# Kernel tuning notes

Hardware: AMD Instinct MI355X
Metric: run time of the kernel (lower is better)

Reference implementation:

```python
import jax, jax.numpy as jnp
import numpy as np

B, S, IN, IN2, H = 512, 256, 300, 300, 512
FN = 3  # filter_num


def setup_inputs() -> dict:
    key = jax.random.key(0)
    ks = jax.random.split(key, 16)
    def n(k, shape, scale=0.05):
        return jax.random.normal(k, shape, dtype=jnp.float32) * scale
    return {
        "x": jax.random.normal(ks[0], (B, S, IN), dtype=jnp.float32),
        "W_in": n(ks[1], (IN, IN2)), "b_in": n(ks[2], (IN2,)),
        "Wih": n(ks[3], (IN2, 4 * H)), "Whh": n(ks[4], (H, 4 * H)),
        "bih": n(ks[5], (4 * H,)), "bhh": n(ks[6], (4 * H,)),
        "Q": n(ks[7], (H, IN2)), "R": n(ks[8], (IN2, H)),
        "Wc3": n(ks[9], (FN, 1, 3, H)), "bc3": n(ks[10], (FN,)),
        "Wc4": n(ks[11], (FN, 1, 4, H)), "bc4": n(ks[12], (FN,)),
        "Wc5": n(ks[13], (FN, 1, 5, H)), "bc5": n(ks[14], (FN,)),
        "W_lin": n(ks[15], (3 * FN, 2)), "b_lin": jnp.zeros((2,), jnp.float32),
    }


def reference(x, W_in, b_in, Wih, Whh, bih, bhh, Q, R,
              Wc3, bc3, Wc4, bc4, Wc5, bc5, W_lin, b_lin):
    # input projection: [B,S,IN] -> [B,S,IN2]
    xin = jnp.tanh(x @ W_in + b_in)
    xs = jnp.swapaxes(xin, 0, 1)  # [S,B,IN2] for scan
    bsz = x.shape[0]
    h0 = jnp.zeros((bsz, H), x.dtype)
    c0 = jnp.zeros((bsz, H), x.dtype)

    def step(carry, xt):
        ht, Ct = carry
        # mogrify, mog_iterations=2: i=1 odd updates x, i=2 even updates h
        xt = 2.0 * jax.nn.sigmoid(ht @ Q) * xt
        ht = 2.0 * jax.nn.sigmoid(xt @ R) * ht
        gates = xt @ Wih + bih + ht @ Whh + bhh  # [B,4H]
        i, f, g, o = jnp.split(gates, 4, axis=1)
        Ct = jax.nn.sigmoid(f) * Ct + jax.nn.sigmoid(i) * jnp.tanh(g)
        ht = jax.nn.sigmoid(o) * jnp.tanh(Ct)
        return (ht, Ct), ht

    _, hs = jax.lax.scan(step, (h0, c0), xs)  # [S,B,H]
    hmap = jnp.swapaxes(hs, 0, 1)[:, None, :, :]  # [B,1,S,H]

    feats = []
    for w, b in ((Wc3, bc3), (Wc4, bc4), (Wc5, bc5)):
        y = jax.lax.conv_general_dilated(
            hmap, w, (1, 1), 'VALID',
            dimension_numbers=('NCHW', 'OIHW', 'NCHW'))
        y = jax.nn.relu(y + b[None, :, None, None])  # [B,FN,S-fsz+1,1]
        feats.append(jnp.max(y, axis=(2, 3)))  # global max pool -> [B,FN]
    cat = jnp.concatenate(feats, axis=1)  # [B, 3*FN]
    # dropout is identity at inference
    return cat @ W_lin + b_lin  # [B,2]
```

## Files before the change

### kernel.cpp

```cpp
#include <hip/hip_runtime.h>

#define DI __device__ __forceinline__

typedef __attribute__((ext_vector_type(4))) float  f32x4;
typedef __attribute__((ext_vector_type(8))) short  s16x8;
typedef __attribute__((ext_vector_type(8))) __bf16 bf16x8;

constexpr int S_   = 256;
constexpr int B_   = 512;
constexpr int H_   = 512;
constexpr int KP_  = 320;
constexpr int ALD_ = 832;
constexpr int NRING = 34;
constexpr int NWG  = 256;
constexpr size_t HSLOT = 512 * 512;

constexpr size_t OFF_XIN = 0;
constexpr size_t SZ_XIN  = (size_t)S_ * B_ * KP_ * 2;
constexpr size_t OFF_U   = OFF_XIN + SZ_XIN;
constexpr size_t SZ_U    = (size_t)B_ * S_ * 64 * 4;
constexpr size_t OFF_HS  = OFF_U + SZ_U;
constexpr size_t SZ_HS   = (size_t)NRING * HSLOT * 2;
constexpr size_t OFF_ACT = OFF_HS + SZ_HS;
constexpr size_t SZ_ACT  = (size_t)B_ * ALD_ * 2;
constexpr size_t OFF_HFP = OFF_ACT + SZ_ACT;
constexpr size_t SZ_HFP  = (size_t)B_ * H_ * 4;
constexpr size_t OFF_WPT = OFF_HFP + SZ_HFP;
constexpr size_t SZ_WPT  = (size_t)320 * 320 * 2;
constexpr size_t OFF_QPT = OFF_WPT + SZ_WPT;
constexpr size_t SZ_QPT  = (size_t)320 * 512 * 2;
constexpr size_t OFF_RPT = OFF_QPT + SZ_QPT;
constexpr size_t SZ_RPT  = (size_t)512 * 320 * 2;
constexpr size_t OFF_WGT = OFF_RPT + SZ_RPT;
constexpr size_t SZ_WGT  = (size_t)2048 * 832 * 2;
constexpr size_t OFF_BG  = OFF_WGT + SZ_WGT;
constexpr size_t SZ_BG   = 2048 * 4;
constexpr size_t OFF_VT  = OFF_BG + SZ_BG;
constexpr size_t SZ_VT   = (size_t)64 * 512 * 2;
constexpr size_t OFF_BAR = OFF_VT + SZ_VT;
constexpr size_t SZ_BAR  = 4096;
constexpr size_t WS_NEED = OFF_BAR + SZ_BAR;

DI unsigned short f2bf(float x) {
  unsigned int u = __float_as_uint(x);
  unsigned int r = (u + 0x7FFFu + ((u >> 16) & 1u)) >> 16;
  return (unsigned short)r;
}
DI float bf2f(unsigned short h) { return __uint_as_float(((unsigned int)h) << 16); }

DI float sigm(float x) {
  float e = __builtin_amdgcn_exp2f(x * -1.44269504088896f);
  return __builtin_amdgcn_rcpf(1.0f + e);
}
DI float tanh_(float x) {
  x = fminf(fmaxf(x, -15.0f), 15.0f);
  float e = __builtin_amdgcn_exp2f(x * 2.88539008177793f);
  return (e - 1.0f) * __builtin_amdgcn_rcpf(e + 1.0f);
}
DI bf16x8 asbf(s16x8 v) { return __builtin_bit_cast(bf16x8, v); }

DI unsigned long long ld_sys_u64(const void* p) {
  return __hip_atomic_load((const unsigned long long*)p, __ATOMIC_RELAXED,
                           __HIP_MEMORY_SCOPE_SYSTEM);
}
DI void st_sys_u64(void* p, unsigned long long v) {
  __hip_atomic_store((unsigned long long*)p, v, __ATOMIC_RELAXED,
                     __HIP_MEMORY_SCOPE_SYSTEM);
}
template<int N> DI void wait_vm() {
  asm volatile("s_waitcnt vmcnt(%0)" :: "n"(N) : "memory");
}

struct a16x8 { unsigned long long lo, hi; };
DI a16x8 ldA(const unsigned short* p) {
  a16x8 r; r.lo = ld_sys_u64(p); r.hi = ld_sys_u64(p + 4); return r;
}
DI void stA_lds(short* dst, a16x8 v) {
  *(unsigned long long*)dst = v.lo; *(unsigned long long*)(dst + 4) = v.hi;
}

template<int NK>
DI void gemm_sys(const unsigned short* Ab, int lda,
                 const unsigned short* Bb, int ldb,
                 short* sA, short* sB, f32x4 acc[2][2])
{
  const int tid  = threadIdx.x;
  const int lane = tid & 63;
  const int w = tid >> 6, wm = w >> 1, wn = w & 1;
  const unsigned short* ga = Ab + (tid >> 2) * lda + (tid & 3) * 8;
  const unsigned short* gb = Bb + (tid >> 2) * ldb + (tid & 3) * 8;
  const int arow0 = (wm * 32 + (lane & 15)) * 32 + (lane >> 4) * 8;
  const int brow0 = (wn * 32 + (lane & 15)) * 32 + (lane >> 4) * 8;

  a16x8 a0 = ldA(ga), a1 = {};
  s16x8 b0 = *(const s16x8*)gb, b1 = {};
  if (NK > 1) { a1 = ldA(ga + 32); b1 = *(const s16x8*)(gb + 32); }
  stA_lds(&sA[tid * 8], a0);
  *(s16x8*)&sB[tid * 8] = b0;
  __syncthreads();
  #pragma unroll
  for (int k = 0; k < NK; ++k) {
    const int cur = (k & 1) * 2048;
    if (k + 2 < NK) {
      if ((k & 1) == 0) { a0 = ldA(ga + (k + 2) * 32); b0 = *(const s16x8*)(gb + (k + 2) * 32); }
      else              { a1 = ldA(ga + (k + 2) * 32); b1 = *(const s16x8*)(gb + (k + 2) * 32); }
    }
    s16x8 A0 = *(const s16x8*)&sA[cur + arow0];
    s16x8 A1 = *(const s16x8*)&sA[cur + arow0 + 16 * 32];
    s16x8 B0 = *(const s16x8*)&sB[cur + brow0];
    s16x8 B1 = *(const s16x8*)&sB[cur + brow0 + 16 * 32];
    acc[0][0] = __builtin_amdgcn_mfma_f32_16x16x32_bf16(asbf(A0), asbf(B0), acc[0][0], 0, 0, 0);
    acc[0][1] = __builtin_amdgcn_mfma_f32_16x16x32_bf16(asbf(A0), asbf(B1), acc[0][1], 0, 0, 0);
    acc[1][0] = __builtin_amdgcn_mfma_f32_16x16x32_bf16(asbf(A1), asbf(B0), acc[1][0], 0, 0, 0);
    acc[1][1] = __builtin_amdgcn_mfma_f32_16x16x32_bf16(asbf(A1), asbf(B1), acc[1][1], 0, 0, 0);
    if (k + 1 < NK) {
      const int nxt = ((k + 1) & 1) * 2048;
      if ((k & 1) == 0) { stA_lds(&sA[nxt + tid * 8], a1); *(s16x8*)&sB[nxt + tid * 8] = b1; }
      else              { stA_lds(&sA[nxt + tid * 8], a0); *(s16x8*)&sB[nxt + tid * 8] = b0; }
    }
    __syncthreads();
  }
}

template<int NK, int KREAL>
DI void gemm_f32A(const float* Af, int lda,
                  const unsigned short* Bb, int ldb,
                  short* sA, short* sB, f32x4 acc[2][2])
{
  const int tid  = threadIdx.x;
  const int lane = tid & 63;
  const int w = tid >> 6, wm = w >> 1, wn = w & 1;
  const float* ga = Af + (tid >> 2) * lda;
  const int cseg  = (tid & 3) * 8;
  const unsigned short* gb = Bb + (tid >> 2) * ldb + (tid & 3) * 8;
  const int arow0 = (wm * 32 + (lane & 15)) * 32 + (lane >> 4) * 8;
  const int brow0 = (wn * 32 + (lane & 15)) * 32 + (lane >> 4) * 8;

  auto loadA = [&](int k) -> s16x8 {
    s16x8 r;
    const int c0 = k * 32 + cseg;
    if (c0 + 8 <= KREAL) {
      float4 f0 = *(const float4*)(ga + c0);
      float4 f1 = *(const float4*)(ga + c0 + 4);
      r[0] = (short)f2bf(f0.x); r[1] = (short)f2bf(f0.y);
      r[2] = (short)f2bf(f0.z); r[3] = (short)f2bf(f0.w);
      r[4] = (short)f2bf(f1.x); r[5] = (short)f2bf(f1.y);
      r[6] = (short)f2bf(f1.z); r[7] = (short)f2bf(f1.w);
    } else {
      #pragma unroll
      for (int j = 0; j < 8; ++j) {
        float x = (c0 + j < KREAL) ? ga[c0 + j] : 0.0f;
        r[j] = (short)f2bf(x);
      }
    }
    return r;
  };

  s16x8 va = loadA(0);
  s16x8 vb = *(const s16x8*)gb;
  *(s16x8*)&sA[tid * 8] = va;
  *(s16x8*)&sB[tid * 8] = vb;
  __syncthreads();
  for (int k = 0; k < NK; ++k) {
    const int cur = (k & 1) * 2048;
    if (k + 1 < NK) {
      va = loadA(k + 1);
      vb = *(const s16x8*)(gb + (k + 1) * 32);
    }
    s16x8 a0 = *(const s16x8*)&sA[cur + arow0];
    s16x8 a1 = *(const s16x8*)&sA[cur + arow0 + 16 * 32];
    s16x8 b0 = *(const s16x8*)&sB[cur + brow0];
    s16x8 b1 = *(const s16x8*)&sB[cur + brow0 + 16 * 32];
    acc[0][0] = __builtin_amdgcn_mfma_f32_16x16x32_bf16(asbf(a0), asbf(b0), acc[0][0], 0, 0, 0);
    acc[0][1] = __builtin_amdgcn_mfma_f32_16x16x32_bf16(asbf(a0), asbf(b1), acc[0][1], 0, 0, 0);
    acc[1][0] = __builtin_amdgcn_mfma_f32_16x16x32_bf16(asbf(a1), asbf(b0), acc[1][0], 0, 0, 0);
    acc[1][1] = __builtin_amdgcn_mfma_f32_16x16x32_bf16(asbf(a1), asbf(b1), acc[1][1], 0, 0, 0);
    if (k + 1 < NK) {
      const int nxt = ((k + 1) & 1) * 2048;
      *(s16x8*)&sA[nxt + tid * 8] = va;
      *(s16x8*)&sB[nxt + tid * 8] = vb;
    }
    __syncthreads();
  }
}

template<typename F>
DI void epiloop(f32x4 acc[2][2], F&& f) {
  const int lane = threadIdx.x & 63;
  const int w = threadIdx.x >> 6, wm = w >> 1, wn = w & 1;
  #pragma unroll
  for (int mi = 0; mi < 2; ++mi)
    #pragma unroll
    for (int ni = 0; ni < 2; ++ni)
      #pragma unroll
      for (int r = 0; r < 4; ++r) {
        const int rowl = wm * 32 + mi * 16 + (lane >> 4) * 4 + r;
        const int coll = wn * 32 + ni * 16 + (lane & 15);
        f(rowl, coll, acc[mi][ni][r]);
      }
}

DI void pack_store_tile(const unsigned short* lds16, unsigned short* dstbase, int ldd) {
  const unsigned long long* l64 = (const unsigned long long*)lds16;
  #pragma unroll
  for (int it = 0; it < 4; ++it) {
    const int i = it * 256 + threadIdx.x;
    const int row = i >> 4, q = i & 15;
    st_sys_u64(dstbase + row * ldd + q * 4, l64[row * 16 + q]);
  }
}

__global__ void k_prep_wpt(const float* __restrict__ Wi, unsigned short* __restrict__ WpT) {
  int i = blockIdx.x * 256 + threadIdx.x;
  if (i >= 320 * 320) return;
  int n = i / 320, k = i % 320;
  float v = (n < 300 && k < 300) ? Wi[k * 300 + n] : 0.0f;
  WpT[i] = f2bf(v);
}
__global__ void k_prep_qpt(const float* __restrict__ Q, unsigned short* __restrict__ QpT) {
  int i = blockIdx.x * 256 + threadIdx.x;
  if (i >= 320 * 512) return;
  int n = i >> 9, k = i & 511;
  float v = (n < 300) ? Q[k * 300 + n] : 0.0f;
  QpT[i] = f2bf(v);
}
__global__ void k_prep_rpt(const float* __restrict__ R, unsigned short* __restrict__ RpT) {
  int i = blockIdx.x * 256 + threadIdx.x;
  if (i >= 512 * 320) return;
  int n = i / 320, k = i % 320;
  float v = (k < 300) ? R[k * 512 + n] : 0.0f;
  RpT[i] = f2bf(v);
}
__global__ void k_prep_wgt(const float* __restrict__ Wih, const float* __restrict__ Whh,
                           unsigned short* __restrict__ WgT) {
  int i = blockIdx.x * 256 + threadIdx.x;
  if (i >= 2048 * 832) return;
  int np = i / 832, k = i % 832;
  int c = np >> 2, g = np & 3, col = g * 512 + c;
  float v = 0.0f;
  if (k < 300) v = Wih[k * 2048 + col];
  else if (k >= 320) v = Whh[(k - 320) * 2048 + col];
  WgT[i] = f2bf(v);
}
__global__ void k_prep_bg(const float* __restrict__ bih, const float* __restrict__ bhh,
                          float* __restrict__ bg) {
  int i = blockIdx.x * 256 + threadIdx.x;
  if (i >= 2048) return;
  int c = i >> 2, g = i & 3, col = g * 512 + c;
  bg[i] = bih[col] + bhh[col];
}
__global__ void k_prep_vt(const float* __restrict__ Wc3, const float* __restrict__ Wc4,
                          const float* __restrict__ Wc5, unsigned short* __restrict__ VT) {
  int i = blockIdx.x * 256 + threadIdx.x;
  if (i >= 64 * 512) return;
  int j = i >> 9, k = i & 511;
  float v = 0.0f;
  if (j < 9)       { int f = j / 3,  dt = j % 3;        v = Wc3[(f * 3 + dt) * 512 + k]; }
  else if (j < 21) { int jj = j - 9;  int f = jj / 4, dt = jj % 4; v = Wc4[(f * 4 + dt) * 512 + k]; }
  else if (j < 36) { int jj = j - 21; int f = jj / 5, dt = jj % 5; v = Wc5[(f * 5 + dt) * 512 + k]; }
  VT[i] = f2bf(v);
}
__global__ void k_wsfail(float* out, int n, float v) {
  int i = blockIdx.x * 256 + threadIdx.x;
  if (i < n) out[i] = -v;
}

__global__ __launch_bounds__(256) void k_proj(const float* __restrict__ x,
                                              const unsigned short* __restrict__ WpT,
                                              const float* __restrict__ b_in,
                                              unsigned short* __restrict__ xin) {
  __shared__ short sA[4096], sB[4096];
  const int m0 = blockIdx.x * 64, n0 = blockIdx.y * 64;
  f32x4 acc[2][2];
  const f32x4 z = {0.f, 0.f, 0.f, 0.f};
  acc[0][0] = z; acc[0][1] = z; acc[1][0] = z; acc[1][1] = z;
  gemm_f32A<10, 300>(x + (size_t)m0 * 300, 300, WpT + n0 * 320, 320, sA, sB, acc);
  epiloop(acc, [&](int rowl, int coll, float vacc) {
    const int row = m0 + rowl, col = n0 + coll;
    float o = 0.0f;
    if (col < 300) o = tanh_(vacc + b_in[col]);
    const int b = row >> 8, s = row & 255;
    xin[(size_t)(s * 512 + b) * KP_ + col] = f2bf(o);
  });
}

__global__ __launch_bounds__(256) void k_scan(
    const unsigned short* __restrict__ xin,
    const unsigned short* __restrict__ QpT,
    const unsigned short* __restrict__ RpT,
    const unsigned short* __restrict__ WgT,
    const float* __restrict__ bg,
    const unsigned short* __restrict__ VT,
    unsigned short* __restrict__ hs,
    unsigned short* __restrict__ act,
    float* __restrict__ hfp,
    float* __restrict__ U,
    unsigned int* __restrict__ bar)
{
  __shared__ short sA[4096], sB[4096];
  __shared__ float gbuf[4096];
  const int wg  = blockIdx.x;
  const int grp = wg >> 5;
  const int l   = wg & 31;
  const int tid = threadIdx.x;
  const f32x4 z = {0.f, 0.f, 0.f, 0.f};

  const int gm0 = grp * 64;
  const int gn0 = l * 64;
  float c_state[4] = {0.f, 0.f, 0.f, 0.f};

  int ep = 0;
  auto bar_sync = [&]() {
    wait_vm<0>();
    __syncthreads();
    if (tid == 0) {
      __hip_atomic_fetch_add(&bar[grp * 64], 1u,
                             __ATOMIC_RELAXED, __HIP_MEMORY_SCOPE_AGENT);
      const unsigned tgt = (unsigned)(ep + 1) * 32u;
      while (__hip_atomic_load(&bar[grp * 64], __ATOMIC_RELAXED,
                               __HIP_MEMORY_SCOPE_AGENT) < tgt)
        __builtin_amdgcn_s_sleep(1);
    }
    __syncthreads();
    ++ep;
  };

  for (int t = 0; t < S_; ++t) {
    const unsigned short* hst = hs + (size_t)(t % NRING) * HSLOT;
    unsigned short*       hso = hs + (size_t)((t + 1) % NRING) * HSLOT;

    if (l < 5) {
      const int m0 = gm0, n0 = l * 64;
      f32x4 acc[2][2];
      acc[0][0] = z; acc[0][1] = z; acc[1][0] = z; acc[1][1] = z;
      gemm_sys<16>(hst + m0 * 512, 512, QpT + n0 * 512, 512, sA, sB, acc);
      const unsigned short* xin_t = xin + (size_t)t * 512 * KP_;
      unsigned short* g16 = (unsigned short*)gbuf;
      epiloop(acc, [&](int rowl, int coll, float vacc) {
        const int row = m0 + rowl, col = n0 + coll;
        g16[rowl * 64 + coll] = f2bf(2.0f * sigm(vacc) * bf2f(xin_t[row * KP_ + col]));
      });
      __syncthreads();
      pack_store_tile(g16, act + m0 * ALD_ + n0, ALD_);
    }
    bar_sync();

    if (l < 8) {
      const int m0 = gm0, n0 = l * 64;
      unsigned long long* g64 = (unsigned long long*)gbuf;
      #pragma unroll
      for (int it = 0; it < 8; ++it) {
        const int i = it * 256 + tid;
        const int row = i >> 5, p = i & 31;
        g64[row * 32 + p] = ld_sys_u64(hfp + (m0 + row) * 512 + n0 + p * 2);
      }
      f32x4 acc[2][2];
      acc[0][0] = z; acc[0][1] = z; acc[1][0] = z; acc[1][1] = z;
      gemm_sys<10>(act + m0 * ALD_, ALD_, RpT + n0 * KP_, KP_, sA, sB, acc);
      unsigned short* g16 = (unsigned short*)sA;
      epiloop(acc, [&](int rowl, int coll, float vacc) {
        g16[rowl * 64 + coll] = f2bf(2.0f * sigm(vacc) * gbuf[rowl * 64 + coll]);
      });
      __syncthreads();
      pack_store_tile(g16, act + m0 * ALD_ + 320 + n0, ALD_);
    }
    bar_sync();

    {
      f32x4 acc[2][2];
      acc[0][0] = z; acc[0][1] = z; acc[1][0] = z; acc[1][1] = z;
      gemm_sys<26>(act + gm0 * ALD_, ALD_, WgT + gn0 * 832, 832, sA, sB, acc);
      epiloop(acc, [&](int rowl, int coll, float vacc) {
        gbuf[rowl * 64 + coll] = vacc;
      });
      unsigned short* hbuf = (unsigned short*)sA;
      float*          fbuf = (float*)sB;
      __syncthreads();
      #pragma unroll
      for (int q = 0; q < 4; ++q) {
        const int item = q * 256 + tid;
        const int row = item >> 4, cu = item & 15;
        const float4 bb = *(const float4*)&bg[gn0 + cu * 4];
        const float iv = gbuf[row * 64 + cu * 4 + 0] + bb.x;
        const float fv = gbuf[row * 64 + cu * 4 + 1] + bb.y;
        const float gv = gbuf[row * 64 + cu * 4 + 2] + bb.z;
        const float ov = gbuf[row * 64 + cu * 4 + 3] + bb.w;
        const float cn = sigm(fv) * c_state[q] + sigm(iv) * tanh_(gv);
        const float h  = sigm(ov) * tanh_(cn);
        c_state[q] = cn;
        hbuf[row * 16 + cu] = f2bf(h);
        fbuf[row * 16 + cu] = h;
      }
      __syncthreads();
      {
        const unsigned long long* h64 = (const unsigned long long*)hbuf;
        const int row = tid >> 2, q = tid & 3;
        st_sys_u64(hso + (gm0 + row) * 512 + (gn0 >> 2) + q * 4, h64[row * 4 + q]);
        const unsigned long long* f64 = (const unsigned long long*)fbuf;
        #pragma unroll
        for (int it = 0; it < 2; ++it) {
          const int i = it * 256 + tid;
          const int r2 = i >> 3, p = i & 7;
          st_sys_u64(hfp + (gm0 + r2) * 512 + (gn0 >> 2) + p * 2, f64[r2 * 8 + p]);
        }
      }
      __syncthreads();
    }
    bar_sync();

    if ((t & 31) == 31) {
      const int c = t >> 5;
      const int tglob = 32 * c + l;
      const int slot = (tglob + 1) % NRING;
      const int brow = gm0;
      f32x4 acc[2][2];
      acc[0][0] = z; acc[0][1] = z; acc[1][0] = z; acc[1][1] = z;
      gemm_sys<16>(hs + (size_t)slot * HSLOT + (size_t)brow * 512, 512, VT, 512, sA, sB, acc);
      epiloop(acc, [&](int rowl, int coll, float vacc) {
        U[((size_t)(brow + rowl) * 256 + tglob) * 64 + coll] = vacc;
      });
    }
  }
}

__global__ __launch_bounds__(256) void k_combine(const float* __restrict__ U,
                                                 const float* __restrict__ bc3,
                                                 const float* __restrict__ bc4,
                                                 const float* __restrict__ bc5,
                                                 const float* __restrict__ Wl,
                                                 const float* __restrict__ bl,
                                                 float* __restrict__ out) {
  const int b = blockIdx.x;
  const int p = threadIdx.x;
  const float* Ub = U + (size_t)b * (256 * 64);
  float v[9];
  #pragma unroll
  for (int j = 0; j < 9; ++j) v[j] = -1e30f;
  if (p < 254) {
    #pragma unroll
    for (int f = 0; f < 3; ++f)
      v[f] = Ub[(p + 0) * 64 + f * 3 + 0] + Ub[(p + 1) * 64 + f * 3 + 1] + Ub[(p + 2) * 64 + f * 3 + 2];
  }
  if (p < 253) {
    #pragma unroll
    for (int f = 0; f < 3; ++f)
      v[3 + f] = Ub[(p + 0) * 64 + 9 + f * 4 + 0] + Ub[(p + 1) * 64 + 9 + f * 4 + 1] +
                 Ub[(p + 2) * 64 + 9 + f * 4 + 2] + Ub[(p + 3) * 64 + 9 + f * 4 + 3];
  }
  if (p < 252) {
    #pragma unroll
    for (int f = 0; f < 3; ++f)
      v[6 + f] = Ub[(p + 0) * 64 + 21 + f * 5 + 0] + Ub[(p + 1) * 64 + 21 + f * 5 + 1] +
                 Ub[(p + 2) * 64 + 21 + f * 5 + 2] + Ub[(p + 3) * 64 + 21 + f * 5 + 3] +
                 Ub[(p + 4) * 64 + 21 + f * 5 + 4];
  }
  __shared__ float red[4][9];
  const int lane = threadIdx.x & 63, w = threadIdx.x >> 6;
  #pragma unroll
  for (int j = 0; j < 9; ++j) {
    float m = v[j];
    #pragma unroll
    for (int off = 32; off >= 1; off >>= 1) m = fmaxf(m, __shfl_xor(m, off));
    if (lane == 0) red[w][j] = m;
  }
  __syncthreads();
  if (threadIdx.x < 2) {
    const int k = threadIdx.x;
    float o = bl[k];
    #pragma unroll
    for (int j = 0; j < 9; ++j) {
      float m = fmaxf(fmaxf(red[0][j], red[1][j]), fmaxf(red[2][j], red[3][j]));
      float bias = (j < 3) ? bc3[j] : (j < 6) ? bc4[j - 3] : bc5[j - 6];
      o += fmaxf(m + bias, 0.0f) * Wl[j * 2 + k];
    }
    out[b * 2 + k] = o;
  }
}

extern "C" void kernel_launch(void* const* d_in, const int* in_sizes, int n_in,
                              void* d_out, int out_size, void* d_ws, size_t ws_size,
                              hipStream_t stream) {
  const float* x     = (const float*)d_in[0];
  const float* W_in  = (const float*)d_in[1];
  const float* b_in  = (const float*)d_in[2];
  const float* Wih   = (const float*)d_in[3];
  const float* Whh   = (const float*)d_in[4];
  const float* bih   = (const float*)d_in[5];
  const float* bhh   = (const float*)d_in[6];
  const float* Q     = (const float*)d_in[7];
  const float* R     = (const float*)d_in[8];
  const float* Wc3   = (const float*)d_in[9];
  const float* bc3   = (const float*)d_in[10];
  const float* Wc4   = (const float*)d_in[11];
  const float* bc4   = (const float*)d_in[12];
  const float* Wc5   = (const float*)d_in[13];
  const float* bc5   = (const float*)d_in[14];
  const float* W_lin = (const float*)d_in[15];
  const float* b_lin = (const float*)d_in[16];

  if (ws_size < WS_NEED) {
    k_wsfail<<<4, 256, 0, stream>>>((float*)d_out, out_size, (float)(ws_size >> 20));
    return;
  }

  char* ws = (char*)d_ws;
  unsigned short* xin = (unsigned short*)(ws + OFF_XIN);
  float*          U   = (float*)(ws + OFF_U);
  unsigned short* hs  = (unsigned short*)(ws + OFF_HS);
  unsigned short* act = (unsigned short*)(ws + OFF_ACT);
  float*          hfp = (float*)(ws + OFF_HFP);
  unsigned short* WpT = (unsigned short*)(ws + OFF_WPT);
  unsigned short* QpT = (unsigned short*)(ws + OFF_QPT);
  unsigned short* RpT = (unsigned short*)(ws + OFF_RPT);
  unsigned short* WgT = (unsigned short*)(ws + OFF_WGT);
  float*          bg  = (float*)(ws + OFF_BG);
  unsigned short* VT  = (unsigned short*)(ws + OFF_VT);
  unsigned int*   bar = (unsigned int*)(ws + OFF_BAR);

  (void)hipMemsetAsync(hs, 0, HSLOT * 2, stream);
  (void)hipMemsetAsync(hfp, 0, SZ_HFP, stream);
  (void)hipMemsetAsync(bar, 0, SZ_BAR, stream);

  k_prep_wpt<<<(320 * 320 + 255) / 256, 256, 0, stream>>>(W_in, WpT);
  k_prep_qpt<<<(320 * 512 + 255) / 256, 256, 0, stream>>>(Q, QpT);
  k_prep_rpt<<<(512 * 320 + 255) / 256, 256, 0, stream>>>(R, RpT);
  k_prep_wgt<<<(2048 * 832 + 255) / 256, 256, 0, stream>>>(Wih, Whh, WgT);
  k_prep_bg<<<8, 256, 0, stream>>>(bih, bhh, bg);
  k_prep_vt<<<(64 * 512 + 255) / 256, 256, 0, stream>>>(Wc3, Wc4, Wc5, VT);

  k_proj<<<dim3(131072 / 64, KP_ / 64), 256, 0, stream>>>(x, WpT, b_in, xin);

  k_scan<<<NWG, 256, 0, stream>>>(xin, QpT, RpT, WgT, bg, VT, hs, act, hfp, U, bar);

  k_combine<<<512, 256, 0, stream>>>(U, bc3, bc4, bc5, W_lin, b_lin, (float*)d_out);
}
```

Before: 6.144 ms.

## Replace counter barrier with per-WG flag barrier and deepen GEMM K-pipeline

The group barrier changes from one atomic counter polled by thread 0 to per-workgroup flag slots. Each workgroup writes its epoch tag, and every wavefront polls all 32 flags with a wave-wide all-reduce, which drops the atomic RMW and the trailing __syncthreads. The small GEMM helper now processes four K-chunks per LDS stage and keeps up to three stages of global loads in flight in registers, so there are far fewer __syncthreads per GEMM inside the sequential scan. The cost is four times the LDS (64KB for sA/sB) and much higher register use, which can cut occupancy or cause spills, plus the flag array must be zeroed and laid out correctly.

```diff
diff --git a/kernel.cpp b/kernel.cpp
--- a/kernel.cpp
+++ b/kernel.cpp
@@ -67,6 +67,12 @@
   __hip_atomic_store((unsigned long long*)p, v, __ATOMIC_RELAXED,
                      __HIP_MEMORY_SCOPE_SYSTEM);
 }
+DI unsigned int ld_sys_u32(const unsigned int* p) {
+  return __hip_atomic_load(p, __ATOMIC_RELAXED, __HIP_MEMORY_SCOPE_SYSTEM);
+}
+DI void st_sys_u32(unsigned int* p, unsigned int v) {
+  __hip_atomic_store(p, v, __ATOMIC_RELAXED, __HIP_MEMORY_SCOPE_SYSTEM);
+}
 template<int N> DI void wait_vm() {
   asm volatile("s_waitcnt vmcnt(%0)" :: "n"(N) : "memory");
 }
@@ -79,11 +85,13 @@
   *(unsigned long long*)dst = v.lo; *(unsigned long long*)(dst + 4) = v.hi;
 }
 
-template<int NK>
-DI void gemm_sys(const unsigned short* Ab, int lda,
-                 const unsigned short* Bb, int ldb,
-                 short* sA, short* sB, f32x4 acc[2][2])
+template<int NK, int KU>
+DI void gemmN(const unsigned short* Ab, int lda,
+              const unsigned short* Bb, int ldb,
+              short* sA, short* sB, f32x4 acc[2][2])
 {
+  constexpr int NR = (NK + KU - 1) / KU;
+  constexpr int RS = KU * 2048;
   const int tid  = threadIdx.x;
   const int lane = tid & 63;
   const int w = tid >> 6, wm = w >> 1, wn = w & 1;
@@ -92,31 +100,49 @@
   const int arow0 = (wm * 32 + (lane & 15)) * 32 + (lane >> 4) * 8;
   const int brow0 = (wn * 32 + (lane & 15)) * 32 + (lane >> 4) * 8;
 
-  a16x8 a0 = ldA(ga), a1 = {};
-  s16x8 b0 = *(const s16x8*)gb, b1 = {};
-  if (NK > 1) { a1 = ldA(ga + 32); b1 = *(const s16x8*)(gb + 32); }
-  stA_lds(&sA[tid * 8], a0);
-  *(s16x8*)&sB[tid * 8] = b0;
+  a16x8 pa[3][KU];
+  s16x8 pb[3][KU];
+  #pragma unroll
+  for (int r = 0; r < 3; ++r)
+    #pragma unroll
+    for (int q = 0; q < KU; ++q) {
+      const int t = r * KU + q;
+      if (t < NK) { pa[r][q] = ldA(ga + t * 32); pb[r][q] = *(const s16x8*)(gb + t * 32); }
+    }
+  #pragma unroll
+  for (int q = 0; q < KU; ++q)
+    if (q < NK) { stA_lds(&sA[q * 2048 + tid * 8], pa[0][q]);
+                  *(s16x8*)&sB[q * 2048 + tid * 8] = pb[0][q]; }
   __syncthreads();
   #pragma unroll
-  for (int k = 0; k < NK; ++k) {
-    const int cur = (k & 1) * 2048;
-    if (k + 2 < NK) {
-      if ((k & 1) == 0) { a0 = ldA(ga + (k + 2) * 32); b0 = *(const s16x8*)(gb + (k + 2) * 32); }
-      else              { a1 = ldA(ga + (k + 2) * 32); b1 = *(const s16x8*)(gb + (k + 2) * 32); }
-    }
-    s16x8 A0 = *(const s16x8*)&sA[cur + arow0];
-    s16x8 A1 = *(const s16x8*)&sA[cur + arow0 + 16 * 32];
-    s16x8 B0 = *(const s16x8*)&sB[cur + brow0];
-    s16x8 B1 = *(const s16x8*)&sB[cur + brow0 + 16 * 32];
-    acc[0][0] = __builtin_amdgcn_mfma_f32_16x16x32_bf16(asbf(A0), asbf(B0), acc[0][0], 0, 0, 0);
-    acc[0][1] = __builtin_amdgcn_mfma_f32_16x16x32_bf16(asbf(A0), asbf(B1), acc[0][1], 0, 0, 0);
-    acc[1][0] = __builtin_amdgcn_mfma_f32_16x16x32_bf16(asbf(A1), asbf(B0), acc[1][0], 0, 0, 0);
-    acc[1][1] = __builtin_amdgcn_mfma_f32_16x16x32_bf16(asbf(A1), asbf(B1), acc[1][1], 0, 0, 0);
-    if (k + 1 < NK) {
-      const int nxt = ((k + 1) & 1) * 2048;
-      if ((k & 1) == 0) { stA_lds(&sA[nxt + tid * 8], a1); *(s16x8*)&sB[nxt + tid * 8] = b1; }
-      else              { stA_lds(&sA[nxt + tid * 8], a0); *(s16x8*)&sB[nxt + tid * 8] = b0; }
+  for (int j = 0; j < NR; ++j) {
+    const int cur = (j & 1) * RS;
+    #pragma unroll
+    for (int q = 0; q < KU; ++q) {
+      const int t = (j + 3) * KU + q;
+      if (t < NK) { pa[j % 3][q] = ldA(ga + t * 32); pb[j % 3][q] = *(const s16x8*)(gb + t * 32); }
+    }
+    #pragma unroll
+    for (int q = 0; q < KU; ++q) {
+      if (j * KU + q < NK) {
+        s16x8 A0 = *(const s16x8*)&sA[cur + q * 2048 + arow0];
+        s16x8 A1 = *(const s16x8*)&sA[cur + q * 2048 + arow0 + 512];
+        s16x8 B0 = *(const s16x8*)&sB[cur + q * 2048 + brow0];
+        s16x8 B1 = *(const s16x8*)&sB[cur + q * 2048 + brow0 + 512];
+        acc[0][0] = __builtin_amdgcn_mfma_f32_16x16x32_bf16(asbf(A0), asbf(B0), acc[0][0], 0, 0, 0);
+        acc[0][1] = __builtin_amdgcn_mfma_f32_16x16x32_bf16(asbf(A0), asbf(B1), acc[0][1], 0, 0, 0);
+        acc[1][0] = __builtin_amdgcn_mfma_f32_16x16x32_bf16(asbf(A1), asbf(B0), acc[1][0], 0, 0, 0);
+        acc[1][1] = __builtin_amdgcn_mfma_f32_16x16x32_bf16(asbf(A1), asbf(B1), acc[1][1], 0, 0, 0);
+      }
+    }
+    if (j + 1 < NR) {
+      const int nxt = ((j + 1) & 1) * RS;
+      #pragma unroll
+      for (int q = 0; q < KU; ++q) {
+        const int t = (j + 1) * KU + q;
+        if (t < NK) { stA_lds(&sA[nxt + q * 2048 + tid * 8], pa[(j + 1) % 3][q]);
+                      *(s16x8*)&sB[nxt + q * 2048 + tid * 8] = pb[(j + 1) % 3][q]; }
+      }
     }
     __syncthreads();
   }
@@ -297,31 +323,28 @@
     float* __restrict__ U,
     unsigned int* __restrict__ bar)
 {
-  __shared__ short sA[4096], sB[4096];
+  __shared__ short sA[16384], sB[16384];
   __shared__ float gbuf[4096];
-  const int wg  = blockIdx.x;
-  const int grp = wg >> 5;
-  const int l   = wg & 31;
-  const int tid = threadIdx.x;
+  const int wg   = blockIdx.x;
+  const int grp  = wg >> 5;
+  const int l    = wg & 31;
+  const int tid  = threadIdx.x;
+  const int lane = tid & 63;
   const f32x4 z = {0.f, 0.f, 0.f, 0.f};
 
   const int gm0 = grp * 64;
   const int gn0 = l * 64;
   float c_state[4] = {0.f, 0.f, 0.f, 0.f};
 
+  unsigned int* flags = bar + grp * 32;
   int ep = 0;
   auto bar_sync = [&]() {
     wait_vm<0>();
     __syncthreads();
-    if (tid == 0) {
-      __hip_atomic_fetch_add(&bar[grp * 64], 1u,
-                             __ATOMIC_RELAXED, __HIP_MEMORY_SCOPE_AGENT);
-      const unsigned tgt = (unsigned)(ep + 1) * 32u;
-      while (__hip_atomic_load(&bar[grp * 64], __ATOMIC_RELAXED,
-                               __HIP_MEMORY_SCOPE_AGENT) < tgt)
-        __builtin_amdgcn_s_sleep(1);
-    }
-    __syncthreads();
+    const unsigned tag = (unsigned)(ep + 1);
+    if (tid == 0) st_sys_u32(&flags[l], tag);
+    while (!__all(ld_sys_u32(&flags[lane & 31]) >= tag))
+      __builtin_amdgcn_s_sleep(2);
     ++ep;
   };
 
@@ -333,7 +356,7 @@
       const int m0 = gm0, n0 = l * 64;
       f32x4 acc[2][2];
       acc[0][0] = z; acc[0][1] = z; acc[1][0] = z; acc[1][1] = z;
-      gemm_sys<16>(hst + m0 * 512, 512, QpT + n0 * 512, 512, sA, sB, acc);
+      gemmN<16, 4>(hst + m0 * 512, 512, QpT + n0 * 512, 512, sA, sB, acc);
       const unsigned short* xin_t = xin + (size_t)t * 512 * KP_;
       unsigned short* g16 = (unsigned short*)gbuf;
       epiloop(acc, [&](int rowl, int coll, float vacc) {
@@ -356,7 +379,7 @@
       }
       f32x4 acc[2][2];
       acc[0][0] = z; acc[0][1] = z; acc[1][0] = z; acc[1][1] = z;
-      gemm_sys<10>(act + m0 * ALD_, ALD_, RpT + n0 * KP_, KP_, sA, sB, acc);
+      gemmN<10, 4>(act + m0 * ALD_, ALD_, RpT + n0 * KP_, KP_, sA, sB, acc);
       unsigned short* g16 = (unsigned short*)sA;
       epiloop(acc, [&](int rowl, int coll, float vacc) {
         g16[rowl * 64 + coll] = f2bf(2.0f * sigm(vacc) * gbuf[rowl * 64 + coll]);
@@ -369,7 +392,7 @@
     {
       f32x4 acc[2][2];
       acc[0][0] = z; acc[0][1] = z; acc[1][0] = z; acc[1][1] = z;
-      gemm_sys<26>(act + gm0 * ALD_, ALD_, WgT + gn0 * 832, 832, sA, sB, acc);
+      gemmN<26, 4>(act + gm0 * ALD_, ALD_, WgT + gn0 * 832, 832, sA, sB, acc);
       epiloop(acc, [&](int rowl, int coll, float vacc) {
         gbuf[rowl * 64 + coll] = vacc;
       });
@@ -415,7 +438,7 @@
       const int brow = gm0;
       f32x4 acc[2][2];
       acc[0][0] = z; acc[0][1] = z; acc[1][0] = z; acc[1][1] = z;
-      gemm_sys<16>(hs + (size_t)slot * HSLOT + (size_t)brow * 512, 512, VT, 512, sA, sB, acc);
+      gemmN<16, 4>(hs + (size_t)slot * HSLOT + (size_t)brow * 512, 512, VT, 512, sA, sB, acc);
       epiloop(acc, [&](int rowl, int coll, float vacc) {
         U[((size_t)(brow + rowl) * 256 + tglob) * 64 + coll] = vacc;
       });
```

Result: slower. 6.912 ms (+12.5%).

## Split-K the per-step scan GEMMs across two 256-thread teams per workgroup

Applied to the files above, without the earlier changes.

The persistent scan kernel now launches 512 threads per workgroup instead of 256. The two halves each take alternating K tiles of every per-step GEMM, then combine their partial accumulators through LDS. This halves the serial K-loop length on the recurrent critical path and adds more waves to hide global-load latency. In exchange it needs more LDS, an extra reduction and barrier per GEMM, and tighter register limits under launch_bounds(512,2).

```diff
diff --git a/kernel.cpp b/kernel.cpp
--- a/kernel.cpp
+++ b/kernel.cpp
@@ -5,6 +5,7 @@
 typedef __attribute__((ext_vector_type(4))) float  f32x4;
 typedef __attribute__((ext_vector_type(8))) short  s16x8;
 typedef __attribute__((ext_vector_type(8))) __bf16 bf16x8;
+typedef unsigned long long u64;
 
 constexpr int S_   = 256;
 constexpr int B_   = 512;
@@ -59,66 +60,96 @@
 }
 DI bf16x8 asbf(s16x8 v) { return __builtin_bit_cast(bf16x8, v); }
 
-DI unsigned long long ld_sys_u64(const void* p) {
-  return __hip_atomic_load((const unsigned long long*)p, __ATOMIC_RELAXED,
-                           __HIP_MEMORY_SCOPE_SYSTEM);
-}
-DI void st_sys_u64(void* p, unsigned long long v) {
-  __hip_atomic_store((unsigned long long*)p, v, __ATOMIC_RELAXED,
-                     __HIP_MEMORY_SCOPE_SYSTEM);
+DI u64 ld_sys_u64(const void* p) {
+  return __hip_atomic_load((const u64*)p, __ATOMIC_RELAXED, __HIP_MEMORY_SCOPE_SYSTEM);
+}
+DI void st_sys_u64(void* p, u64 v) {
+  __hip_atomic_store((u64*)p, v, __ATOMIC_RELAXED, __HIP_MEMORY_SCOPE_SYSTEM);
 }
 template<int N> DI void wait_vm() {
   asm volatile("s_waitcnt vmcnt(%0)" :: "n"(N) : "memory");
 }
 
-struct a16x8 { unsigned long long lo, hi; };
+struct a16x8 { u64 lo, hi; };
 DI a16x8 ldA(const unsigned short* p) {
   a16x8 r; r.lo = ld_sys_u64(p); r.hi = ld_sys_u64(p + 4); return r;
 }
 DI void stA_lds(short* dst, a16x8 v) {
-  *(unsigned long long*)dst = v.lo; *(unsigned long long*)(dst + 4) = v.hi;
-}
-
-template<int NK>
-DI void gemm_sys(const unsigned short* Ab, int lda,
-                 const unsigned short* Bb, int ldb,
-                 short* sA, short* sB, f32x4 acc[2][2])
+  *(u64*)dst = v.lo; *(u64*)(dst + 4) = v.hi;
+}
+
+template<int NR>
+DI void gemm2(const unsigned short* Ab, int lda,
+              const unsigned short* Bb, int ldb,
+              short* sA, short* sB, f32x4 acc[2][2])
 {
   const int tid  = threadIdx.x;
-  const int lane = tid & 63;
-  const int w = tid >> 6, wm = w >> 1, wn = w & 1;
-  const unsigned short* ga = Ab + (tid >> 2) * lda + (tid & 3) * 8;
-  const unsigned short* gb = Bb + (tid >> 2) * ldb + (tid & 3) * 8;
+  const int t2   = tid & 255;
+  const int team = tid >> 8;
+  const int lane = t2 & 63;
+  const int w = t2 >> 6, wm = w >> 1, wn = w & 1;
+  const unsigned short* ga = Ab + (t2 >> 2) * lda + (t2 & 3) * 8;
+  const unsigned short* gb = Bb + (t2 >> 2) * ldb + (t2 & 3) * 8;
+  const int slot  = team * 2048;
   const int arow0 = (wm * 32 + (lane & 15)) * 32 + (lane >> 4) * 8;
   const int brow0 = (wn * 32 + (lane & 15)) * 32 + (lane >> 4) * 8;
 
-  a16x8 a0 = ldA(ga), a1 = {};
-  s16x8 b0 = *(const s16x8*)gb, b1 = {};
-  if (NK > 1) { a1 = ldA(ga + 32); b1 = *(const s16x8*)(gb + 32); }
-  stA_lds(&sA[tid * 8], a0);
-  *(s16x8*)&sB[tid * 8] = b0;
+  a16x8 a0, a1 = {};
+  s16x8 b0, b1 = {};
+  a0 = ldA(ga + team * 32);
+  b0 = *(const s16x8*)(gb + team * 32);
+  if (NR > 1) {
+    a1 = ldA(ga + (2 + team) * 32);
+    b1 = *(const s16x8*)(gb + (2 + team) * 32);
+  }
+  stA_lds(&sA[slot + t2 * 8], a0);
+  *(s16x8*)&sB[slot + t2 * 8] = b0;
   __syncthreads();
   #pragma unroll
-  for (int k = 0; k < NK; ++k) {
-    const int cur = (k & 1) * 2048;
-    if (k + 2 < NK) {
-      if ((k & 1) == 0) { a0 = ldA(ga + (k + 2) * 32); b0 = *(const s16x8*)(gb + (k + 2) * 32); }
-      else              { a1 = ldA(ga + (k + 2) * 32); b1 = *(const s16x8*)(gb + (k + 2) * 32); }
-    }
-    s16x8 A0 = *(const s16x8*)&sA[cur + arow0];
-    s16x8 A1 = *(const s16x8*)&sA[cur + arow0 + 16 * 32];
-    s16x8 B0 = *(const s16x8*)&sB[cur + brow0];
-    s16x8 B1 = *(const s16x8*)&sB[cur + brow0 + 16 * 32];
+  for (int j = 0; j < NR; ++j) {
+    const int cur = (j & 1) * 4096;
+    if (j + 2 < NR) {
+      const int kt = 2 * (j + 2) + team;
+      if ((j & 1) == 0) { a0 = ldA(ga + kt * 32); b0 = *(const s16x8*)(gb + kt * 32); }
+      else              { a1 = ldA(ga + kt * 32); b1 = *(const s16x8*)(gb + kt * 32); }
+    }
+    s16x8 A0 = *(const s16x8*)&sA[cur + slot + arow0];
+    s16x8 A1 = *(const s16x8*)&sA[cur + slot + arow0 + 512];
+    s16x8 B0 = *(const s16x8*)&sB[cur + slot + brow0];
+    s16x8 B1 = *(const s16x8*)&sB[cur + slot + brow0 + 512];
     acc[0][0] = __builtin_amdgcn_mfma_f32_16x16x32_bf16(asbf(A0), asbf(B0), acc[0][0], 0, 0, 0);
     acc[0][1] = __builtin_amdgcn_mfma_f32_16x16x32_bf16(asbf(A0), asbf(B1), acc[0][1], 0, 0, 0);
     acc[1][0] = __builtin_amdgcn_mfma_f32_16x16x32_bf16(asbf(A1), asbf(B0), acc[1][0], 0, 0, 0);
     acc[1][1] = __builtin_amdgcn_mfma_f32_16x16x32_bf16(asbf(A1), asbf(B1), acc[1][1], 0, 0, 0);
-    if (k + 1 < NK) {
-      const int nxt = ((k + 1) & 1) * 2048;
-      if ((k & 1) == 0) { stA_lds(&sA[nxt + tid * 8], a1); *(s16x8*)&sB[nxt + tid * 8] = b1; }
-      else              { stA_lds(&sA[nxt + tid * 8], a0); *(s16x8*)&sB[nxt + tid * 8] = b0; }
+    if (j + 1 < NR) {
+      const int nxt = ((j + 1) & 1) * 4096;
+      if ((j & 1) == 0) { stA_lds(&sA[nxt + slot + t2 * 8], a1); *(s16x8*)&sB[nxt + slot + t2 * 8] = b1; }
+      else              { stA_lds(&sA[nxt + slot + t2 * 8], a0); *(s16x8*)&sB[nxt + slot + t2 * 8] = b0; }
     }
     __syncthreads();
+  }
+}
+
+DI void reduce_teams(f32x4 acc[2][2], float* rbuf) {
+  const int tid = threadIdx.x, t2 = tid & 255;
+  if (tid >= 256) {
+    #pragma unroll
+    for (int mi = 0; mi < 2; ++mi)
+      #pragma unroll
+      for (int ni = 0; ni < 2; ++ni)
+        #pragma unroll
+        for (int r = 0; r < 4; ++r)
+          rbuf[((mi * 2 + ni) * 4 + r) * 256 + t2] = acc[mi][ni][r];
+  }
+  __syncthreads();
+  if (tid < 256) {
+    #pragma unroll
+    for (int mi = 0; mi < 2; ++mi)
+      #pragma unroll
+      for (int ni = 0; ni < 2; ++ni)
+        #pragma unroll
+        for (int r = 0; r < 4; ++r)
+          acc[mi][ni][r] += rbuf[((mi * 2 + ni) * 4 + r) * 256 + t2];
   }
 }
 
@@ -187,7 +218,7 @@
 template<typename F>
 DI void epiloop(f32x4 acc[2][2], F&& f) {
   const int lane = threadIdx.x & 63;
-  const int w = threadIdx.x >> 6, wm = w >> 1, wn = w & 1;
+  const int w = (threadIdx.x & 255) >> 6, wm = w >> 1, wn = w & 1;
   #pragma unroll
   for (int mi = 0; mi < 2; ++mi)
     #pragma unroll
@@ -200,11 +231,11 @@
       }
 }
 
-DI void pack_store_tile(const unsigned short* lds16, unsigned short* dstbase, int ldd) {
-  const unsigned long long* l64 = (const unsigned long long*)lds16;
+DI void pack_store_512(const unsigned short* lds16, unsigned short* dstbase, int ldd) {
+  const u64* l64 = (const u64*)lds16;
   #pragma unroll
-  for (int it = 0; it < 4; ++it) {
-    const int i = it * 256 + threadIdx.x;
+  for (int it = 0; it < 2; ++it) {
+    const int i = it * 512 + threadIdx.x;
     const int row = i >> 4, q = i & 15;
     st_sys_u64(dstbase + row * ldd + q * 4, l64[row * 16 + q]);
   }
@@ -284,7 +315,7 @@
   });
 }
 
-__global__ __launch_bounds__(256) void k_scan(
+__global__ __launch_bounds__(512, 2) void k_scan(
     const unsigned short* __restrict__ xin,
     const unsigned short* __restrict__ QpT,
     const unsigned short* __restrict__ RpT,
@@ -297,17 +328,20 @@
     float* __restrict__ U,
     unsigned int* __restrict__ bar)
 {
-  __shared__ short sA[4096], sB[4096];
+  __shared__ short sA[8192], sB[8192];
   __shared__ float gbuf[4096];
-  const int wg  = blockIdx.x;
-  const int grp = wg >> 5;
-  const int l   = wg & 31;
-  const int tid = threadIdx.x;
+  __shared__ float rbuf[4096];
+  __shared__ float pbuf[4096];
+  __shared__ unsigned short obuf[4096];
+  const int wg   = blockIdx.x;
+  const int grp  = wg >> 5;
+  const int l    = wg & 31;
+  const int tid  = threadIdx.x;
   const f32x4 z = {0.f, 0.f, 0.f, 0.f};
 
   const int gm0 = grp * 64;
   const int gn0 = l * 64;
-  float c_state[4] = {0.f, 0.f, 0.f, 0.f};
+  float c_state[2] = {0.f, 0.f};
 
   int ep = 0;
   auto bar_sync = [&]() {
@@ -333,52 +367,61 @@
       const int m0 = gm0, n0 = l * 64;
       f32x4 acc[2][2];
       acc[0][0] = z; acc[0][1] = z; acc[1][0] = z; acc[1][1] = z;
-      gemm_sys<16>(hst + m0 * 512, 512, QpT + n0 * 512, 512, sA, sB, acc);
-      const unsigned short* xin_t = xin + (size_t)t * 512 * KP_;
-      unsigned short* g16 = (unsigned short*)gbuf;
-      epiloop(acc, [&](int rowl, int coll, float vacc) {
-        const int row = m0 + rowl, col = n0 + coll;
-        g16[rowl * 64 + coll] = f2bf(2.0f * sigm(vacc) * bf2f(xin_t[row * KP_ + col]));
-      });
+      gemm2<8>(hst + m0 * 512, 512, QpT + n0 * 512, 512, sA, sB, acc);
+      reduce_teams(acc, rbuf);
+      if (tid < 256) {
+        const unsigned short* xin_t = xin + (size_t)t * 512 * KP_;
+        epiloop(acc, [&](int rowl, int coll, float vacc) {
+          obuf[rowl * 64 + coll] =
+            f2bf(2.0f * sigm(vacc) * bf2f(xin_t[(m0 + rowl) * KP_ + n0 + coll]));
+        });
+      }
       __syncthreads();
-      pack_store_tile(g16, act + m0 * ALD_ + n0, ALD_);
+      pack_store_512(obuf, act + m0 * ALD_ + n0, ALD_);
     }
     bar_sync();
 
     if (l < 8) {
       const int m0 = gm0, n0 = l * 64;
-      unsigned long long* g64 = (unsigned long long*)gbuf;
-      #pragma unroll
-      for (int it = 0; it < 8; ++it) {
-        const int i = it * 256 + tid;
-        const int row = i >> 5, p = i & 31;
-        g64[row * 32 + p] = ld_sys_u64(hfp + (m0 + row) * 512 + n0 + p * 2);
+      {
+        u64* p64 = (u64*)pbuf;
+        #pragma unroll
+        for (int it = 0; it < 4; ++it) {
+          const int i = it * 512 + tid;
+          const int row = i >> 5, p = i & 31;
+          p64[row * 32 + p] = ld_sys_u64(hfp + (m0 + row) * 512 + n0 + p * 2);
+        }
       }
       f32x4 acc[2][2];
       acc[0][0] = z; acc[0][1] = z; acc[1][0] = z; acc[1][1] = z;
-      gemm_sys<10>(act + m0 * ALD_, ALD_, RpT + n0 * KP_, KP_, sA, sB, acc);
-      unsigned short* g16 = (unsigned short*)sA;
-      epiloop(acc, [&](int rowl, int coll, float vacc) {
-        g16[rowl * 64 + coll] = f2bf(2.0f * sigm(vacc) * gbuf[rowl * 64 + coll]);
-      });
+      gemm2<5>(act + m0 * ALD_, ALD_, RpT + n0 * KP_, KP_, sA, sB, acc);
+      reduce_teams(acc, rbuf);
+      if (tid < 256) {
+        epiloop(acc, [&](int rowl, int coll, float vacc) {
+          obuf[rowl * 64 + coll] = f2bf(2.0f * sigm(vacc) * pbuf[rowl * 64 + coll]);
+        });
+      }
       __syncthreads();
-      pack_store_tile(g16, act + m0 * ALD_ + 320 + n0, ALD_);
+      pack_store_512(obuf, act + m0 * ALD_ + 320 + n0, ALD_);
     }
     bar_sync();
 
     {
       f32x4 acc[2][2];
       acc[0][0] = z; acc[0][1] = z; acc[1][0] = z; acc[1][1] = z;
-      gemm_sys<26>(act + gm0 * ALD_, ALD_, WgT + gn0 * 832, 832, sA, sB, acc);
-      epiloop(acc, [&](int rowl, int coll, float vacc) {
-        gbuf[rowl * 64 + coll] = vacc;
-      });
-      unsigned short* hbuf = (unsigned short*)sA;
-      float*          fbuf = (float*)sB;
+      gemm2<13>(act + gm0 * ALD_, ALD_, WgT + gn0 * 832, 832, sA, sB, acc);
+      reduce_teams(acc, rbuf);
+      if (tid < 256) {
+        epiloop(acc, [&](int rowl, int coll, float vacc) {
+          gbuf[rowl * 64 + coll] = vacc;
+        });
+      }
       __syncthreads();
+      unsigned short* hbuf = obuf;
+      float*          fbuf = rbuf;
       #pragma unroll
-      for (int q = 0; q < 4; ++q) {
-        const int item = q * 256 + tid;
+      for (int q = 0; q < 2; ++q) {
+        const int item = q * 512 + tid;
         const int row = item >> 4, cu = item & 15;
         const float4 bb = *(const float4*)&bg[gn0 + cu * 4];
         const float iv = gbuf[row * 64 + cu * 4 + 0] + bb.x;
@@ -392,19 +435,16 @@
         fbuf[row * 16 + cu] = h;
       }
       __syncthreads();
-      {
-        const unsigned long long* h64 = (const unsigned long long*)hbuf;
+      if (tid < 256) {
+        const u64* h64 = (const u64*)hbuf;
         const int row = tid >> 2, q = tid & 3;
         st_sys_u64(hso + (gm0 + row) * 512 + (gn0 >> 2) + q * 4, h64[row * 4 + q]);
-        const unsigned long long* f64 = (const unsigned long long*)fbuf;
-        #pragma unroll
-        for (int it = 0; it < 2; ++it) {
-          const int i = it * 256 + tid;
-          const int r2 = i >> 3, p = i & 7;
-          st_sys_u64(hfp + (gm0 + r2) * 512 + (gn0 >> 2) + p * 2, f64[r2 * 8 + p]);
-        }
-      }
-      __syncthreads();
+      }
+      {
+        const u64* f64 = (const u64*)fbuf;
+        const int r2 = tid >> 3, p = tid & 7;
+        st_sys_u64(hfp + (gm0 + r2) * 512 + (gn0 >> 2) + p * 2, f64[r2 * 8 + p]);
+      }
     }
     bar_sync();
 
@@ -415,10 +455,13 @@
       const int brow = gm0;
       f32x4 acc[2][2];
       acc[0][0] = z; acc[0][1] = z; acc[1][0] = z; acc[1][1] = z;
-      gemm_sys<16>(hs + (size_t)slot * HSLOT + (size_t)brow * 512, 512, VT, 512, sA, sB, acc);
-      epiloop(acc, [&](int rowl, int coll, float vacc) {
-        U[((size_t)(brow + rowl) * 256 + tglob) * 64 + coll] = vacc;
-      });
+      gemm2<8>(hs + (size_t)slot * HSLOT + (size_t)brow * 512, 512, VT, 512, sA, sB, acc);
+      reduce_teams(acc, rbuf);
+      if (tid < 256) {
+        epiloop(acc, [&](int rowl, int coll, float vacc) {
+          U[((size_t)(brow + rowl) * 256 + tglob) * 64 + coll] = vacc;
+        });
+      }
     }
   }
 }
@@ -530,7 +573,7 @@
 
   k_proj<<<dim3(131072 / 64, KP_ / 64), 256, 0, stream>>>(x, WpT, b_in, xin);
 
-  k_scan<<<NWG, 256, 0, stream>>>(xin, QpT, RpT, WgT, bg, VT, hs, act, hfp, U, bar);
+  k_scan<<<NWG, 512, 0, stream>>>(xin, QpT, RpT, WgT, bg, VT, hs, act, hfp, U, bar);
 
   k_combine<<<512, 256, 0, stream>>>(U, bc3, bc4, bc5, W_lin, b_lin, (float*)d_out);
 }
```

After: 5.490 ms. 10.7% less time.
